# Kernel optimization log

Hardware: AMD Instinct MI355X
Metric: run time of the kernel (lower is better)

## Reference

```python
import jax, jax.numpy as jnp
import numpy as np

N_NODES = 50000
N_EDGES = 800000
IN_CH = 128
HID_CH = 256  # 2 * out_channels
OUT_CH = 128


def setup_inputs() -> dict:
    key = jax.random.key(0)
    ks = jax.random.split(key, 8)
    x = jax.random.normal(ks[0], (N_NODES, IN_CH), dtype=jnp.float32)
    edge_index = jax.random.randint(ks[1], (2, N_EDGES), 0, N_NODES, dtype=jnp.int64)
    batch = jnp.zeros((N_NODES,), dtype=jnp.int64)
    # GCNConv weights (PyG: glorot init; here random normal scaled)
    W1 = jax.random.normal(ks[2], (IN_CH, HID_CH), dtype=jnp.float32) / np.sqrt(IN_CH)
    b1 = jnp.zeros((HID_CH,), dtype=jnp.float32)
    W2 = jax.random.normal(ks[3], (HID_CH, OUT_CH), dtype=jnp.float32) / np.sqrt(HID_CH)
    b2 = jnp.zeros((OUT_CH,), dtype=jnp.float32)
    return {"x": x, "edge_index": edge_index, "batch": batch,
            "W1": W1, "b1": b1, "W2": W2, "b2": b2}


def _gcn_norm(edge_index, num_nodes):
    # add self-loops, compute symmetric normalization (PyG GCNConv default)
    loop = jnp.arange(num_nodes, dtype=edge_index.dtype)
    src = jnp.concatenate([edge_index[0], loop])
    dst = jnp.concatenate([edge_index[1], loop])
    deg = jax.ops.segment_sum(jnp.ones_like(dst, dtype=jnp.float32), dst,
                              num_segments=num_nodes)
    dis = jnp.where(deg > 0, jax.lax.rsqrt(deg), 0.0)  # deg^{-1/2}, inf->0
    norm = dis[src] * dis[dst]  # [E+N]
    return src, dst, norm


def _gcn_conv(x, W, b, src, dst, norm, num_nodes):
    h = x @ W                              # [N, F_out] dense GEMM
    msg = h[src] * norm[:, None]           # gather + per-edge scale
    out = jax.ops.segment_sum(msg, dst, num_segments=num_nodes)  # scatter-add
    return out + b


def reference(x, edge_index, batch, W1, b1, W2, b2):
    n = x.shape[0]
    src, dst, norm = _gcn_norm(edge_index, n)
    h = jax.nn.relu(_gcn_conv(x, W1, b1, src, dst, norm, n))
    h = jax.nn.relu(_gcn_conv(h, W2, b2, src, dst, norm, n))
    return h
```

## Files before the change

kernel.cpp:

```cpp
#include <hip/hip_runtime.h>

#define N_NODES 50000
#define N_EDGES 800000
#define IN_CH 128
#define HID_CH 256
#define OUT_CH 128

constexpr int TOTAL_E = N_EDGES + N_NODES;
constexpr int NBKT = 196;
constexpr int NBLK_BIN = 128;
constexpr int EPB_BIN = N_EDGES / NBLK_BIN;
constexpr int CNT2D = NBKT * NBLK_BIN;
constexpr int SCAN_BLK = 1024;
constexpr int NB_SC = (CNT2D + SCAN_BLK - 1) / SCAN_BLK;
constexpr int COLCAP = 5376;

typedef __attribute__((ext_vector_type(8))) short bf16x8;
typedef __attribute__((ext_vector_type(4))) float f32x4;
typedef __attribute__((ext_vector_type(4))) unsigned int u32x4;


__device__ __forceinline__ unsigned int bf16rn(float x) {
    unsigned int u = __float_as_uint(x);
    return (u + 0x7fffu + ((u >> 16) & 1u)) >> 16;
}

__device__ __forceinline__ void split2(float x0, float x1,
                                       unsigned int& h, unsigned int& l) {
    unsigned int h0 = bf16rn(x0), h1 = bf16rn(x1);
    float f0 = __uint_as_float(h0 << 16), f1 = __uint_as_float(h1 << 16);
    unsigned int l0 = bf16rn(x0 - f0), l1 = bf16rn(x1 - f1);
    h = h0 | (h1 << 16);
    l = l0 | (l1 << 16);
}

__device__ __forceinline__ bf16x8 asbf(u32x4 v) {
    return __builtin_bit_cast(bf16x8, v);
}


__global__ void k_tobf(const float* __restrict__ x, unsigned short* __restrict__ xb,
                       int n8) {
    int i = blockIdx.x * blockDim.x + threadIdx.x;
    if (i >= n8) return;
    const float4* p = (const float4*)(x + (size_t)i * 8);
    float4 a = p[0], b = p[1];
    u32x4 w;
    w.x = bf16rn(a.x) | (bf16rn(a.y) << 16);
    w.y = bf16rn(a.z) | (bf16rn(a.w) << 16);
    w.z = bf16rn(b.x) | (bf16rn(b.y) << 16);
    w.w = bf16rn(b.z) | (bf16rn(b.w) << 16);
    *(u32x4*)(xb + (size_t)i * 8) = w;
}


__global__ __launch_bounds__(256)
void k_count(const int* __restrict__ dst, int* __restrict__ cnt2D) {
    __shared__ int h[NBKT];
    int b = blockIdx.x, t = threadIdx.x;
    if (t < NBKT) h[t] = 0;
    __syncthreads();
    int e0 = b * EPB_BIN;
    for (int i = t; i < EPB_BIN; i += 256)
        atomicAdd(&h[dst[e0 + i] >> 8], 1);
    __syncthreads();
    if (t < NBKT) cnt2D[t * NBLK_BIN + b] = h[t];
}

__global__ void k_scan1(const int* __restrict__ cnt, int* __restrict__ incl,
                        int* __restrict__ part, int n) {
    __shared__ int s[SCAN_BLK];
    int t = threadIdx.x;
    int i = blockIdx.x * SCAN_BLK + t;
    int v = (i < n) ? cnt[i] : 0;
    s[t] = v; __syncthreads();
    for (int o = 1; o < SCAN_BLK; o <<= 1) {
        int a = (t >= o) ? s[t - o] : 0;
        __syncthreads();
        s[t] += a;
        __syncthreads();
    }
    if (i < n) incl[i] = s[t];
    if (t == SCAN_BLK - 1) part[blockIdx.x] = s[t];
}

__global__ void k_scan2(int* __restrict__ part, int n) {
    __shared__ int s[SCAN_BLK];
    int t = threadIdx.x;
    int v = (t < n) ? part[t] : 0;
    s[t] = v; __syncthreads();
    for (int o = 1; o < SCAN_BLK; o <<= 1) {
        int a = (t >= o) ? s[t - o] : 0;
        __syncthreads();
        s[t] += a;
        __syncthreads();
    }
    if (t < n) part[t] = s[t] - v;
}

__global__ void k_off(int* __restrict__ incl, const int* __restrict__ cnt,
                      const int* __restrict__ part, int n, int total) {
    int i = blockIdx.x * blockDim.x + threadIdx.x;
    if (i < n)       incl[i] = part[i >> 10] + incl[i] - cnt[i];
    else if (i == n) incl[i] = total;
}

__global__ __launch_bounds__(256)
void k_bin(const int* __restrict__ src, const int* __restrict__ dst,
           const int* __restrict__ off2D, int2* __restrict__ binned) {
    __shared__ int cur[NBKT];
    int b = blockIdx.x, t = threadIdx.x;
    if (t < NBKT) cur[t] = off2D[t * NBLK_BIN + b];
    __syncthreads();
    int e0 = b * EPB_BIN;
    for (int i = t; i < EPB_BIN; i += 256) {
        int d = dst[e0 + i];
        int pos = atomicAdd(&cur[d >> 8], 1);
        int2 p; p.x = src[e0 + i]; p.y = d;
        binned[pos] = p;
    }
}

__global__ __launch_bounds__(256)
void k_csr(const int2* __restrict__ binned, const int* __restrict__ off2D,
           int* __restrict__ col, int* __restrict__ off, float* __restrict__ dis) {
    __shared__ int cnt[256], sc[256], cur[256];
    __shared__ int colL[COLCAP];
    int kb = blockIdx.x, t = threadIdx.x;
    int base2 = off2D[kb * NBLK_BIN];
    int end2  = off2D[(kb + 1) * NBLK_BIN];
    int nE = end2 - base2;
    int nn = min(256, N_NODES - kb * 256);
    cnt[t] = 0;
    __syncthreads();
    for (int i = t; i < nE; i += 256)
        atomicAdd(&cnt[binned[base2 + i].y & 255], 1);
    __syncthreads();
    sc[t] = cnt[t];
    __syncthreads();
    for (int o = 1; o < 256; o <<= 1) {
        int a = (t >= o) ? sc[t - o] : 0;
        __syncthreads();
        sc[t] += a;
        __syncthreads();
    }
    int excl = sc[t] - cnt[t];
    cur[t] = excl + t;
    __syncthreads();
    for (int i = t; i < nE; i += 256) {
        int2 p = binned[base2 + i];
        colL[atomicAdd(&cur[p.y & 255], 1)] = p.x;
    }
    __syncthreads();
    int v = kb * 256 + t;
    if (t < nn) {
        colL[cur[t]] = v;
        off[v] = base2 + kb * 256 + excl + t;
        dis[v] = rsqrtf((float)(cnt[t] + 1));
    }
    if (kb == NBKT - 1 && t == 0) off[N_NODES] = TOTAL_E;
    __syncthreads();
    int tot = nE + nn, gbase = base2 + kb * 256;
    for (int i = t; i < tot; i += 256)
        col[gbase + i] = colL[i];
}


template<bool BIAS, bool RELU>
__global__ __launch_bounds__(256)
void k_agg_bf(const unsigned short* __restrict__ featb, const int* __restrict__ col,
              const int* __restrict__ off, const float* __restrict__ dis,
              const float* __restrict__ bias, float* __restrict__ out) {
    int wid  = threadIdx.x >> 6;
    int lane = threadIdx.x & 63;
    int v = blockIdx.x * 4 + wid;
    int start = off[v];
    int lenv  = off[v + 1] - start;
    float disv = dis[v];
    int half = lane >> 5;
    int q    = lane & 31;
    float4 acc = make_float4(0.f, 0.f, 0.f, 0.f);
    for (int base = 0; base < lenv; base += 64) {
        int n = min(64, lenv - base);
        int   cv = 0;
        float wv = 0.f;
        if (lane < n) {
            cv = col[start + base + lane];
            wv = dis[cv] * disv;
        }
        auto pair = [&](int j) {
            int   c = __shfl(cv, j + half);
            float w = __shfl(wv, j + half);
            uint2 d = *(const uint2*)&featb[(size_t)c * 128 + q * 4];
            acc.x = fmaf(w, __uint_as_float(d.x << 16),         acc.x);
            acc.y = fmaf(w, __uint_as_float(d.x & 0xffff0000u), acc.y);
            acc.z = fmaf(w, __uint_as_float(d.y << 16),         acc.z);
            acc.w = fmaf(w, __uint_as_float(d.y & 0xffff0000u), acc.w);
        };
        int j = 0;
        for (; j + 8 <= n; j += 8) { pair(j); pair(j + 2); pair(j + 4); pair(j + 6); }
        for (; j < n; j += 2) pair(j);
    }
    acc.x += __shfl_xor(acc.x, 32);
    acc.y += __shfl_xor(acc.y, 32);
    acc.z += __shfl_xor(acc.z, 32);
    acc.w += __shfl_xor(acc.w, 32);
    if (half == 0) {
        float4 o = acc;
        if (BIAS) {
            float4 b = *(const float4*)&bias[q * 4];
            o.x += b.x; o.y += b.y; o.z += b.z; o.w += b.w;
        }
        if (RELU) {
            o.x = fmaxf(o.x, 0.f); o.y = fmaxf(o.y, 0.f);
            o.z = fmaxf(o.z, 0.f); o.w = fmaxf(o.w, 0.f);
        }
        *(float4*)&out[(size_t)v * 128 + q * 4] = o;
    }
}


template<int K, int NC>
__device__ __forceinline__ void wsplit_body(const float* __restrict__ W,
                                            u32x4* __restrict__ Wf, int tid) {
    constexpr int NT = NC / 16;
    int lane = tid & 63;
    int ntk  = tid >> 6;
    int kt = ntk / NT, nt = ntk % NT;
    int kb = kt * 32 + (lane >> 4) * 8;
    int n  = nt * 16 + (lane & 15);
    unsigned int hh[4], ll[4];
    #pragma unroll
    for (int j = 0; j < 4; ++j) {
        float x0 = W[(size_t)(kb + 2 * j) * NC + n];
        float x1 = W[(size_t)(kb + 2 * j + 1) * NC + n];
        split2(x0, x1, hh[j], ll[j]);
    }
    Wf[(size_t)(ntk * 2 + 0) * 64 + lane] = (u32x4){hh[0], hh[1], hh[2], hh[3]};
    Wf[(size_t)(ntk * 2 + 1) * 64 + lane] = (u32x4){ll[0], ll[1], ll[2], ll[3]};
}

__global__ void k_wsplit_both(const float* __restrict__ W1, u32x4* __restrict__ Wf1,
                              const float* __restrict__ W2, u32x4* __restrict__ Wf2) {
    int tid = blockIdx.x * blockDim.x + threadIdx.x;
    if (tid < 4096)      wsplit_body<IN_CH,  HID_CH>(W1, Wf1, tid);
    else if (tid < 8192) wsplit_body<HID_CH, OUT_CH>(W2, Wf2, tid - 4096);
}


__global__ __launch_bounds__(128)
void k_gemm_fused(const float* __restrict__ A, const u32x4* __restrict__ Wf1,
                  const float* __restrict__ b1, const u32x4* __restrict__ Wf2,
                  unsigned short* __restrict__ outb, int M) {
    __shared__ unsigned short hh[32 * 256];
    __shared__ unsigned short hl[32 * 256];
    int lane = threadIdx.x & 63, wid = threadIdx.x >> 6;
    int lq = lane >> 4, lr = lane & 15, kq = lq * 8;
    int rbase = blockIdx.x * 32;

    f32x4 acc[2][8];
    #pragma unroll
    for (int s = 0; s < 2; ++s)
        #pragma unroll
        for (int t = 0; t < 8; ++t) acc[s][t] = (f32x4){0.f, 0.f, 0.f, 0.f};

    for (int kt = 0; kt < 4; ++kt) {
        bf16x8 ah[2], al[2];
        #pragma unroll
        for (int s = 0; s < 2; ++s) {
            int row = rbase + s * 16 + lr;
            const float* Ar = A + (size_t)min(row, M - 1) * IN_CH + kt * 32 + kq;
            float4 u = *(const float4*)Ar;
            float4 v = *(const float4*)(Ar + 4);
            unsigned int h0, l0, h1, l1, h2, l2, h3, l3;
            split2(u.x, u.y, h0, l0); split2(u.z, u.w, h1, l1);
            split2(v.x, v.y, h2, l2); split2(v.z, v.w, h3, l3);
            ah[s] = asbf((u32x4){h0, h1, h2, h3});
            al[s] = asbf((u32x4){l0, l1, l2, l3});
        }
        #pragma unroll
        for (int t = 0; t < 8; ++t) {
            int nt = wid * 8 + t;
            const u32x4* wp = Wf1 + (size_t)((kt * 16 + nt) * 2) * 64 + lane;
            bf16x8 bh = asbf(wp[0]);
            bf16x8 bl = asbf(wp[64]);
            acc[0][t] = __builtin_amdgcn_mfma_f32_16x16x32_bf16(ah[0], bh, acc[0][t], 0, 0, 0);
            acc[1][t] = __builtin_amdgcn_mfma_f32_16x16x32_bf16(ah[1], bh, acc[1][t], 0, 0, 0);
            acc[0][t] = __builtin_amdgcn_mfma_f32_16x16x32_bf16(al[0], bh, acc[0][t], 0, 0, 0);
            acc[1][t] = __builtin_amdgcn_mfma_f32_16x16x32_bf16(al[1], bh, acc[1][t], 0, 0, 0);
            acc[0][t] = __builtin_amdgcn_mfma_f32_16x16x32_bf16(ah[0], bl, acc[0][t], 0, 0, 0);
            acc[1][t] = __builtin_amdgcn_mfma_f32_16x16x32_bf16(ah[1], bl, acc[1][t], 0, 0, 0);
        }
    }

    #pragma unroll
    for (int t = 0; t < 8; ++t) {
        int colg = (wid * 8 + t) * 16 + lr;
        float bv = b1[colg];
        #pragma unroll
        for (int s = 0; s < 2; ++s) {
            #pragma unroll
            for (int j = 0; j < 4; ++j) {
                int row = s * 16 + lq * 4 + j;
                float o = fmaxf(acc[s][t][j] + bv, 0.f);
                unsigned int hi = bf16rn(o);
                float rem = o - __uint_as_float(hi << 16);
                unsigned int lo = bf16rn(rem);
                int e = (row * 256 + colg) ^ ((row & 7) << 3);
                hh[e] = (unsigned short)hi;
                hl[e] = (unsigned short)lo;
            }
        }
    }
    __syncthreads();

    f32x4 acc2[2][4];
    #pragma unroll
    for (int s = 0; s < 2; ++s)
        #pragma unroll
        for (int t = 0; t < 4; ++t) acc2[s][t] = (f32x4){0.f, 0.f, 0.f, 0.f};

    for (int kt = 0; kt < 8; ++kt) {
        bf16x8 ah[2], al[2];
        #pragma unroll
        for (int s = 0; s < 2; ++s) {
            int row = s * 16 + lr;
            int e = (row * 256 + kt * 32 + kq) ^ ((row & 7) << 3);
            ah[s] = *(const bf16x8*)&hh[e];
            al[s] = *(const bf16x8*)&hl[e];
        }
        #pragma unroll
        for (int t = 0; t < 4; ++t) {
            int nt = wid * 4 + t;
            const u32x4* wp = Wf2 + (size_t)((kt * 8 + nt) * 2) * 64 + lane;
            bf16x8 bh = asbf(wp[0]);
            bf16x8 bl = asbf(wp[64]);
            acc2[0][t] = __builtin_amdgcn_mfma_f32_16x16x32_bf16(ah[0], bh, acc2[0][t], 0, 0, 0);
            acc2[1][t] = __builtin_amdgcn_mfma_f32_16x16x32_bf16(ah[1], bh, acc2[1][t], 0, 0, 0);
            acc2[0][t] = __builtin_amdgcn_mfma_f32_16x16x32_bf16(al[0], bh, acc2[0][t], 0, 0, 0);
            acc2[1][t] = __builtin_amdgcn_mfma_f32_16x16x32_bf16(al[1], bh, acc2[1][t], 0, 0, 0);
            acc2[0][t] = __builtin_amdgcn_mfma_f32_16x16x32_bf16(ah[0], bl, acc2[0][t], 0, 0, 0);
            acc2[1][t] = __builtin_amdgcn_mfma_f32_16x16x32_bf16(ah[1], bl, acc2[1][t], 0, 0, 0);
        }
    }

    #pragma unroll
    for (int t = 0; t < 4; ++t) {
        int colg = (wid * 4 + t) * 16 + lr;
        #pragma unroll
        for (int s = 0; s < 2; ++s) {
            #pragma unroll
            for (int j = 0; j < 4; ++j) {
                int row = rbase + s * 16 + lq * 4 + j;
                if (row < M)
                    outb[(size_t)row * OUT_CH + colg] =
                        (unsigned short)bf16rn(acc2[s][t][j]);
            }
        }
    }
}


extern "C" void kernel_launch(void* const* d_in, const int* in_sizes, int n_in,
                              void* d_out, int out_size, void* d_ws, size_t ws_size,
                              hipStream_t stream) {
    const float* x   = (const float*)d_in[0];
    const int*   ei  = (const int*)d_in[1];
    const int*   src = ei;
    const int*   dst = ei + N_EDGES;
    const float* W1  = (const float*)d_in[3];
    const float* b1  = (const float*)d_in[4];
    const float* W2  = (const float*)d_in[5];
    const float* b2  = (const float*)d_in[6];
    float* out = (float*)d_out;

    char* ws = (char*)d_ws;
    size_t o = 0;
    auto carve = [&](size_t bytes) {
        void* p = ws + o;
        o += (bytes + 255) & ~(size_t)255;
        return p;
    };
    int*   cnt2D  = (int*)  carve((size_t)CNT2D * 4);
    int*   incl2D = (int*)  carve((size_t)(CNT2D + 1) * 4);
    int*   part   = (int*)  carve(SCAN_BLK * 4);
    int*   off    = (int*)  carve((size_t)(N_NODES + 1) * 4);
    float* dis    = (float*)carve(N_NODES * 4);
    int*   col    = (int*)  carve((size_t)TOTAL_E * 4);
    float* agg1   = (float*)carve((size_t)N_NODES * 128 * 4);
    unsigned short* bfbuf = (unsigned short*)carve((size_t)N_NODES * 128 * 2);
    u32x4* Wf1    = (u32x4*)carve((size_t)4 * 16 * 2 * 64 * 16);
    u32x4* Wf2    = (u32x4*)carve((size_t)8 * 8 * 2 * 64 * 16);
    int*   off2D  = incl2D;
    int2*           binned = (int2*)agg1;
    unsigned short* xb     = bfbuf;
    unsigned short* t2b    = bfbuf;

    const int B = 256;
    k_tobf  <<<(N_NODES * 128 / 8 + B - 1) / B, B, 0, stream>>>(x, xb, N_NODES * 128 / 8);
    k_count <<<NBLK_BIN, 256, 0, stream>>>(dst, cnt2D);
    k_scan1 <<<NB_SC, SCAN_BLK, 0, stream>>>(cnt2D, incl2D, part, CNT2D);
    k_scan2 <<<1, SCAN_BLK, 0, stream>>>(part, NB_SC);
    k_off   <<<(CNT2D + 1 + B - 1) / B, B, 0, stream>>>(incl2D, cnt2D, part, CNT2D, N_EDGES);
    k_bin   <<<NBLK_BIN, 256, 0, stream>>>(src, dst, off2D, binned);
    k_csr   <<<NBKT, 256, 0, stream>>>(binned, off2D, col, off, dis);
    k_wsplit_both<<<32, 256, 0, stream>>>(W1, Wf1, W2, Wf2);

    k_agg_bf<false, false><<<N_NODES / 4, 256, 0, stream>>>(xb, col, off, dis, nullptr, agg1);
    k_gemm_fused<<<(N_NODES + 31) / 32, 128, 0, stream>>>(agg1, Wf1, b1, Wf2, t2b, N_NODES);
    k_agg_bf<true, true><<<N_NODES / 4, 256, 0, stream>>>(t2b, col, off, dis, b2, out);
}
```

Measured before the change: 165.7 us.

## Store first aggregation in bf16 and drop A-side split in fused GEMM

The first aggregation now writes bf16 instead of fp32, which halves that intermediate's write and read traffic. The fused GEMM reads bf16 activations directly and removes the low-part split for activations in both GEMMs. That cuts the MFMA count from six to four per tile and frees the second LDS buffer. The block grows to 256 threads, so each wave covers fewer output tiles. The cost is lower precision on the activations, which are now single bf16 while the weights keep their hi/lo split.

```diff
diff --git a/kernel.cpp b/kernel.cpp
--- a/kernel.cpp
+++ b/kernel.cpp
@@ -166,11 +166,11 @@
 }
 
 
-template<bool BIAS, bool RELU>
+template<bool BIAS, bool RELU, bool BF16OUT>
 __global__ __launch_bounds__(256)
 void k_agg_bf(const unsigned short* __restrict__ featb, const int* __restrict__ col,
               const int* __restrict__ off, const float* __restrict__ dis,
-              const float* __restrict__ bias, float* __restrict__ out) {
+              const float* __restrict__ bias, void* __restrict__ outv) {
     int wid  = threadIdx.x >> 6;
     int lane = threadIdx.x & 63;
     int v = blockIdx.x * 4 + wid;
@@ -215,7 +215,14 @@
             o.x = fmaxf(o.x, 0.f); o.y = fmaxf(o.y, 0.f);
             o.z = fmaxf(o.z, 0.f); o.w = fmaxf(o.w, 0.f);
         }
-        *(float4*)&out[(size_t)v * 128 + q * 4] = o;
+        if (BF16OUT) {
+            uint2 p;
+            p.x = bf16rn(o.x) | (bf16rn(o.y) << 16);
+            p.y = bf16rn(o.z) | (bf16rn(o.w) << 16);
+            *(uint2*)&((unsigned short*)outv)[(size_t)v * 128 + q * 4] = p;
+        } else {
+            *(float4*)&((float*)outv)[(size_t)v * 128 + q * 4] = o;
+        }
     }
 }
 
@@ -248,54 +255,44 @@
 }
 
 
-__global__ __launch_bounds__(128)
-void k_gemm_fused(const float* __restrict__ A, const u32x4* __restrict__ Wf1,
+__global__ __launch_bounds__(256)
+void k_gemm_fused(const unsigned short* __restrict__ Ab, const u32x4* __restrict__ Wf1,
                   const float* __restrict__ b1, const u32x4* __restrict__ Wf2,
                   unsigned short* __restrict__ outb, int M) {
     __shared__ unsigned short hh[32 * 256];
-    __shared__ unsigned short hl[32 * 256];
     int lane = threadIdx.x & 63, wid = threadIdx.x >> 6;
     int lq = lane >> 4, lr = lane & 15, kq = lq * 8;
     int rbase = blockIdx.x * 32;
 
-    f32x4 acc[2][8];
+    f32x4 acc[2][4];
     #pragma unroll
     for (int s = 0; s < 2; ++s)
         #pragma unroll
-        for (int t = 0; t < 8; ++t) acc[s][t] = (f32x4){0.f, 0.f, 0.f, 0.f};
+        for (int t = 0; t < 4; ++t) acc[s][t] = (f32x4){0.f, 0.f, 0.f, 0.f};
 
     for (int kt = 0; kt < 4; ++kt) {
-        bf16x8 ah[2], al[2];
+        bf16x8 ah[2];
         #pragma unroll
         for (int s = 0; s < 2; ++s) {
-            int row = rbase + s * 16 + lr;
-            const float* Ar = A + (size_t)min(row, M - 1) * IN_CH + kt * 32 + kq;
-            float4 u = *(const float4*)Ar;
-            float4 v = *(const float4*)(Ar + 4);
-            unsigned int h0, l0, h1, l1, h2, l2, h3, l3;
-            split2(u.x, u.y, h0, l0); split2(u.z, u.w, h1, l1);
-            split2(v.x, v.y, h2, l2); split2(v.z, v.w, h3, l3);
-            ah[s] = asbf((u32x4){h0, h1, h2, h3});
-            al[s] = asbf((u32x4){l0, l1, l2, l3});
-        }
-        #pragma unroll
-        for (int t = 0; t < 8; ++t) {
-            int nt = wid * 8 + t;
+            int row = min(rbase + s * 16 + lr, M - 1);
+            ah[s] = *(const bf16x8*)&Ab[(size_t)row * IN_CH + kt * 32 + kq];
+        }
+        #pragma unroll
+        for (int t = 0; t < 4; ++t) {
+            int nt = wid * 4 + t;
             const u32x4* wp = Wf1 + (size_t)((kt * 16 + nt) * 2) * 64 + lane;
             bf16x8 bh = asbf(wp[0]);
             bf16x8 bl = asbf(wp[64]);
             acc[0][t] = __builtin_amdgcn_mfma_f32_16x16x32_bf16(ah[0], bh, acc[0][t], 0, 0, 0);
             acc[1][t] = __builtin_amdgcn_mfma_f32_16x16x32_bf16(ah[1], bh, acc[1][t], 0, 0, 0);
-            acc[0][t] = __builtin_amdgcn_mfma_f32_16x16x32_bf16(al[0], bh, acc[0][t], 0, 0, 0);
-            acc[1][t] = __builtin_amdgcn_mfma_f32_16x16x32_bf16(al[1], bh, acc[1][t], 0, 0, 0);
             acc[0][t] = __builtin_amdgcn_mfma_f32_16x16x32_bf16(ah[0], bl, acc[0][t], 0, 0, 0);
             acc[1][t] = __builtin_amdgcn_mfma_f32_16x16x32_bf16(ah[1], bl, acc[1][t], 0, 0, 0);
         }
     }
 
     #pragma unroll
-    for (int t = 0; t < 8; ++t) {
-        int colg = (wid * 8 + t) * 16 + lr;
+    for (int t = 0; t < 4; ++t) {
+        int colg = (wid * 4 + t) * 16 + lr;
         float bv = b1[colg];
         #pragma unroll
         for (int s = 0; s < 2; ++s) {
@@ -303,50 +300,43 @@
             for (int j = 0; j < 4; ++j) {
                 int row = s * 16 + lq * 4 + j;
                 float o = fmaxf(acc[s][t][j] + bv, 0.f);
-                unsigned int hi = bf16rn(o);
-                float rem = o - __uint_as_float(hi << 16);
-                unsigned int lo = bf16rn(rem);
                 int e = (row * 256 + colg) ^ ((row & 7) << 3);
-                hh[e] = (unsigned short)hi;
-                hl[e] = (unsigned short)lo;
+                hh[e] = (unsigned short)bf16rn(o);
             }
         }
     }
     __syncthreads();
 
-    f32x4 acc2[2][4];
+    f32x4 acc2[2][2];
     #pragma unroll
     for (int s = 0; s < 2; ++s)
         #pragma unroll
-        for (int t = 0; t < 4; ++t) acc2[s][t] = (f32x4){0.f, 0.f, 0.f, 0.f};
+        for (int t = 0; t < 2; ++t) acc2[s][t] = (f32x4){0.f, 0.f, 0.f, 0.f};
 
     for (int kt = 0; kt < 8; ++kt) {
-        bf16x8 ah[2], al[2];
+        bf16x8 ah[2];
         #pragma unroll
         for (int s = 0; s < 2; ++s) {
             int row = s * 16 + lr;
             int e = (row * 256 + kt * 32 + kq) ^ ((row & 7) << 3);
             ah[s] = *(const bf16x8*)&hh[e];
-            al[s] = *(const bf16x8*)&hl[e];
-        }
-        #pragma unroll
-        for (int t = 0; t < 4; ++t) {
-            int nt = wid * 4 + t;
+        }
+        #pragma unroll
+        for (int t = 0; t < 2; ++t) {
+            int nt = wid * 2 + t;
             const u32x4* wp = Wf2 + (size_t)((kt * 8 + nt) * 2) * 64 + lane;
             bf16x8 bh = asbf(wp[0]);
             bf16x8 bl = asbf(wp[64]);
             acc2[0][t] = __builtin_amdgcn_mfma_f32_16x16x32_bf16(ah[0], bh, acc2[0][t], 0, 0, 0);
             acc2[1][t] = __builtin_amdgcn_mfma_f32_16x16x32_bf16(ah[1], bh, acc2[1][t], 0, 0, 0);
-            acc2[0][t] = __builtin_amdgcn_mfma_f32_16x16x32_bf16(al[0], bh, acc2[0][t], 0, 0, 0);
-            acc2[1][t] = __builtin_amdgcn_mfma_f32_16x16x32_bf16(al[1], bh, acc2[1][t], 0, 0, 0);
             acc2[0][t] = __builtin_amdgcn_mfma_f32_16x16x32_bf16(ah[0], bl, acc2[0][t], 0, 0, 0);
             acc2[1][t] = __builtin_amdgcn_mfma_f32_16x16x32_bf16(ah[1], bl, acc2[1][t], 0, 0, 0);
         }
     }
 
     #pragma unroll
-    for (int t = 0; t < 4; ++t) {
-        int colg = (wid * 4 + t) * 16 + lr;
+    for (int t = 0; t < 2; ++t) {
+        int colg = (wid * 2 + t) * 16 + lr;
         #pragma unroll
         for (int s = 0; s < 2; ++s) {
             #pragma unroll
@@ -387,12 +377,13 @@
     int*   off    = (int*)  carve((size_t)(N_NODES + 1) * 4);
     float* dis    = (float*)carve(N_NODES * 4);
     int*   col    = (int*)  carve((size_t)TOTAL_E * 4);
-    float* agg1   = (float*)carve((size_t)N_NODES * 128 * 4);
+    char*  buf1   = (char*) carve((size_t)N_NODES * 128 * 2);
     unsigned short* bfbuf = (unsigned short*)carve((size_t)N_NODES * 128 * 2);
     u32x4* Wf1    = (u32x4*)carve((size_t)4 * 16 * 2 * 64 * 16);
     u32x4* Wf2    = (u32x4*)carve((size_t)8 * 8 * 2 * 64 * 16);
     int*   off2D  = incl2D;
-    int2*           binned = (int2*)agg1;
+    int2*           binned = (int2*)buf1;
+    unsigned short* agg1b  = (unsigned short*)buf1;
     unsigned short* xb     = bfbuf;
     unsigned short* t2b    = bfbuf;
 
@@ -406,7 +397,9 @@
     k_csr   <<<NBKT, 256, 0, stream>>>(binned, off2D, col, off, dis);
     k_wsplit_both<<<32, 256, 0, stream>>>(W1, Wf1, W2, Wf2);
 
-    k_agg_bf<false, false><<<N_NODES / 4, 256, 0, stream>>>(xb, col, off, dis, nullptr, agg1);
-    k_gemm_fused<<<(N_NODES + 31) / 32, 128, 0, stream>>>(agg1, Wf1, b1, Wf2, t2b, N_NODES);
-    k_agg_bf<true, true><<<N_NODES / 4, 256, 0, stream>>>(t2b, col, off, dis, b2, out);
-}
+    k_agg_bf<false, false, true><<<N_NODES / 4, 256, 0, stream>>>(
+        xb, col, off, dis, nullptr, agg1b);
+    k_gemm_fused<<<(N_NODES + 31) / 32, 256, 0, stream>>>(agg1b, Wf1, b1, Wf2, t2b, N_NODES);
+    k_agg_bf<true, true, false><<<N_NODES / 4, 256, 0, stream>>>(
+        t2b, col, off, dis, b2, out);
+}
```

Result: faster. 150.9 us, median of 2 (-8.9%).
